# Kernel optimization log

Hardware: AMD Instinct MI355X
Metric: run time of the kernel (lower is better)

Reference implementation:

```python
import jax, jax.numpy as jnp
import numpy as np

D_MODEL = 1024
NHEAD = 16
HEAD_DIM = D_MODEL // NHEAD
MAX_LEN = 4096
ROPE_BASE = 500.0


def _rope_tables(L, dim):
    inv_freq = 1.0 / (ROPE_BASE ** (jnp.arange(0, dim, 2, dtype=jnp.float32) / dim))
    t = jnp.arange(L, dtype=jnp.float32)
    freqs = jnp.einsum('i,j->ij', t, inv_freq)  # [L, dim/2]
    emb = jnp.concatenate([freqs, freqs], axis=-1)  # [L, dim]
    return jnp.cos(emb), jnp.sin(emb)


def _rotate_half(x):
    x1, x2 = jnp.split(x, 2, axis=-1)
    return jnp.concatenate([-x2, x1], axis=-1)


def _apply_rope(x, cos, sin):
    return x * cos + _rotate_half(x) * sin


def setup_inputs() -> dict:
    key = jax.random.key(0)
    ks = jax.random.split(key, 6)
    B, L = 4, 2048
    bound_qkv = 1.0 / np.sqrt(D_MODEL)
    x = jax.random.normal(ks[0], (B, L, D_MODEL), dtype=jnp.float32)
    key_padding_mask = jnp.zeros((B, L), dtype=bool)
    W_qkv = jax.random.uniform(ks[1], (3 * D_MODEL, D_MODEL), jnp.float32, -bound_qkv, bound_qkv)
    b_qkv = jax.random.uniform(ks[2], (3 * D_MODEL,), jnp.float32, -bound_qkv, bound_qkv)
    W_out = jax.random.uniform(ks[3], (D_MODEL, D_MODEL), jnp.float32, -bound_qkv, bound_qkv)
    b_out = jax.random.uniform(ks[4], (D_MODEL,), jnp.float32, -bound_qkv, bound_qkv)
    return {"x": x, "key_padding_mask": key_padding_mask,
            "W_qkv": W_qkv, "b_qkv": b_qkv, "W_out": W_out, "b_out": b_out}


def reference(x, key_padding_mask, W_qkv, b_qkv, W_out, b_out):
    B, L, D = x.shape
    H, hd = NHEAD, HEAD_DIM
    qkv = x @ W_qkv.T + b_qkv  # [B, L, 3D]
    q, k, v = jnp.split(qkv, 3, axis=-1)
    # [B, H, L, hd]
    q = q.reshape(B, L, H, hd).transpose(0, 2, 1, 3)
    k = k.reshape(B, L, H, hd).transpose(0, 2, 1, 3)
    v = v.reshape(B, L, H, hd).transpose(0, 2, 1, 3)
    cos, sin = _rope_tables(L, hd)  # [L, hd]
    q = _apply_rope(q, cos, sin)
    k = _apply_rope(k, cos, sin)
    scores = jnp.einsum('bhqd,bhkd->bhqk', q, k) / jnp.sqrt(jnp.float32(hd))
    mask = key_padding_mask[:, None, None, :]  # [B,1,1,L]
    scores = jnp.where(mask, -jnp.inf, scores)
    attn = jax.nn.softmax(scores, axis=-1)
    out = jnp.einsum('bhqk,bhkd->bhqd', attn, v)
    out = out.transpose(0, 2, 1, 3).reshape(B, L, D)
    return out @ W_out.T + b_out
```

## Files before the change

kernel.cpp:

```cpp
#include <hip/hip_runtime.h>
#include <stdint.h>

typedef __attribute__((ext_vector_type(8))) __bf16 bf16x8;
typedef __attribute__((ext_vector_type(4))) short short4v;
typedef __attribute__((ext_vector_type(4))) float f32x4;

#if __has_builtin(__builtin_amdgcn_exp2f)
#define EXP2(x) __builtin_amdgcn_exp2f(x)
#else
#define EXP2(x) exp2f(x)
#endif

__device__ __forceinline__ short f2bf(float f) {
  union { float f; uint32_t u; } v; v.f = f;
  uint32_t r = (v.u + 0x7fffu + ((v.u >> 16) & 1u)) >> 16;
  return (short)(uint16_t)r;
}

__device__ __forceinline__ uint32_t pk2bf(float a, float b) {
  union { __bf16 h; uint16_t u; } x, y;
  x.h = (__bf16)a; y.h = (__bf16)b;
  return (uint32_t)x.u | ((uint32_t)y.u << 16);
}

__device__ __forceinline__ void gl2lds16(const void* g, const void* lds) {
  __builtin_amdgcn_global_load_lds(
      (const __attribute__((address_space(1))) void*)(uintptr_t)g,
      (__attribute__((address_space(3))) void*)(uint32_t)(uintptr_t)lds,
      16, 0, 0);
}

__device__ __forceinline__ bf16x8 frag8(const short* p) {
  return *(const bf16x8*)(const void*)p;
}

__global__ void convert3_k(const float* __restrict__ s0, short* __restrict__ d0, int n0,
                           const float* __restrict__ s1, short* __restrict__ d1, int n1,
                           const float* __restrict__ s2, short* __restrict__ d2, int n2) {
  int i = blockIdx.x * blockDim.x + threadIdx.x;
  int t0 = n0 >> 2, t1 = t0 + (n1 >> 2), t2 = t1 + (n2 >> 2);
  const float* s; short* d; int off;
  if (i < t0) { s = s0; d = d0; off = i; }
  else if (i < t1) { s = s1; d = d1; off = i - t0; }
  else if (i < t2) { s = s2; d = d2; off = i - t1; }
  else return;
  float4 v = ((const float4*)s)[off];
  short4v o;
  o.x = f2bf(v.x); o.y = f2bf(v.y); o.z = f2bf(v.z); o.w = f2bf(v.w);
  *(short4v*)(d + off * 4) = o;
}

__global__ void rope_tab_k(float* __restrict__ cosT, float* __restrict__ sinT,
                           const unsigned char* __restrict__ mask, float* __restrict__ maskf) {
  int i = blockIdx.x * blockDim.x + threadIdx.x;
  int pos = i >> 5, j = i & 31;
  float invf = exp2f(-(float)j * (8.965784284662087f / 32.0f));
  float ang = (float)pos * invf;
  float s, c;
  sincosf(ang, &s, &c);
  cosT[i] = c; sinT[i] = s;
  if (i < 8192) maskf[i] = mask[i] ? -1e30f : 0.0f;
}

template <int EPI>
__global__ __launch_bounds__(256, 3)
void gemm_bt_k(const short* __restrict__ A, const short* __restrict__ Bm,
               const float* __restrict__ bias, int N, int K,
               float* __restrict__ Cout,
               const float* __restrict__ cosT, const float* __restrict__ sinT,
               short* __restrict__ Qb, short* __restrict__ Kb, short* __restrict__ Vt) {
  __shared__ short As[2][128 * 32];
  __shared__ short Bs[2][128 * 32];
  const int tid = threadIdx.x;
  const int lane = tid & 63;
  const int w = tid >> 6;
  const int g = lane >> 4, l15 = lane & 15;
  const int wm = (w >> 1) * 64, wn = (w & 1) * 64;
  const int bm = blockIdx.x, bn = blockIdx.y;

  const int rseg = lane >> 2;
  const int cofs = ((lane & 3) ^ ((lane >> 3) & 3)) * 8;
  const int sA0 = w, sA1 = w + 4;
  const int arow0 = (bm * 128 + sA0 * 16 + rseg) * K;
  const int arow1 = (bm * 128 + sA1 * 16 + rseg) * K;
  const int brow0 = (bn * 128 + sA0 * 16 + rseg) * K;
  const int brow1 = (bn * 128 + sA1 * 16 + rseg) * K;

  const int rsw = (l15 >> 1) & 3;

  f32x4 acc[4][4];
#pragma unroll
  for (int i = 0; i < 4; i++)
#pragma unroll
    for (int j = 0; j < 4; j++) acc[i][j] = f32x4{0.f, 0.f, 0.f, 0.f};

  gl2lds16(A + arow0 + cofs, &As[0][sA0 * 512]);
  gl2lds16(A + arow1 + cofs, &As[0][sA1 * 512]);
  gl2lds16(Bm + brow0 + cofs, &Bs[0][sA0 * 512]);
  gl2lds16(Bm + brow1 + cofs, &Bs[0][sA1 * 512]);

  int cur = 0;
  for (int k0 = 0; k0 < K; k0 += 32, cur ^= 1) {
    __syncthreads();
    int nxt = cur ^ 1;
    int k1 = k0 + 32;
    if (k1 < K) {
      gl2lds16(A + arow0 + k1 + cofs, &As[nxt][sA0 * 512]);
      gl2lds16(A + arow1 + k1 + cofs, &As[nxt][sA1 * 512]);
      gl2lds16(Bm + brow0 + k1 + cofs, &Bs[nxt][sA0 * 512]);
      gl2lds16(Bm + brow1 + k1 + cofs, &Bs[nxt][sA1 * 512]);
    }
    bf16x8 af[4], bf[4];
#pragma unroll
    for (int im = 0; im < 4; im++) af[im] = frag8(&As[cur][(wm + im * 16 + l15) * 32 + (g ^ rsw) * 8]);
#pragma unroll
    for (int jn = 0; jn < 4; jn++) bf[jn] = frag8(&Bs[cur][(wn + jn * 16 + l15) * 32 + (g ^ rsw) * 8]);
#pragma unroll
    for (int im = 0; im < 4; im++)
#pragma unroll
      for (int jn = 0; jn < 4; jn++)
        acc[im][jn] = __builtin_amdgcn_mfma_f32_16x16x32_bf16(af[im], bf[jn], acc[im][jn], 0, 0, 0);
  }

  const int row0 = bm * 128 + wm + g * 4;
  const int col0 = bn * 128 + wn;

  if (EPI == 0) {
#pragma unroll
    for (int jn = 0; jn < 4; jn++) {
      float bb = bias[col0 + jn * 16 + l15];
#pragma unroll
      for (int im = 0; im < 4; im++)
#pragma unroll
        for (int r = 0; r < 4; r++) {
          int row = row0 + im * 16 + r;
          Cout[row * N + col0 + jn * 16 + l15] = acc[im][jn][r] + bb;
        }
    }
  } else {
#pragma unroll
    for (int jn = 0; jn < 4; jn++) {
      float bb = bias[col0 + jn * 16 + l15];
#pragma unroll
      for (int im = 0; im < 4; im++)
#pragma unroll
        for (int r = 0; r < 4; r++) acc[im][jn][r] += bb;
    }
    const int sector = col0 >> 10;
    const int h = (col0 & 1023) >> 6;
    if (sector == 2) {
#pragma unroll
      for (int jn = 0; jn < 4; jn++) {
        int d = jn * 16 + l15;
#pragma unroll
        for (int im = 0; im < 4; im++) {
          int row = row0 + im * 16;
          int b = row >> 11, pos = row & 2047;
          union { uint32_t u[2]; short4v s4; } pw;
          pw.u[0] = pk2bf(acc[im][jn][0], acc[im][jn][1]);
          pw.u[1] = pk2bf(acc[im][jn][2], acc[im][jn][3]);
          *(short4v*)&Vt[((b * 16 + h) * 64 + d) * 2048 + pos] = pw.s4;
        }
      }
    } else {
      short* dst = (sector == 0) ? Qb : Kb;
      const float scl = (sector == 0) ? 0.18033688011112042f : 1.0f;
#pragma unroll
      for (int jn = 0; jn < 4; jn++) {
        int d = jn * 16 + l15;
        int j = d & 31;
#pragma unroll
        for (int im = 0; im < 4; im++)
#pragma unroll
          for (int r = 0; r < 4; r++) {
            int row = row0 + im * 16 + r;
            int b = row >> 11, pos = row & 2047;
            float c = cosT[pos * 32 + j];
            float s = sinT[pos * 32 + j];
            float xv = acc[im][jn][r];
            float xp = acc[im][jn ^ 2][r];
            float rot = (jn < 2) ? -xp : xp;
            dst[((b * 16 + h) * 2048 + pos) * 64 + d] = f2bf((xv * c + rot * s) * scl);
          }
      }
    }
  }
}

__global__ __launch_bounds__(256, 4)
void attn_k(const short* __restrict__ Qb, const short* __restrict__ Kb,
            const short* __restrict__ Vt, const float* __restrict__ maskf,
            short* __restrict__ attn) {
  __shared__ short Ks[3][32 * 64];
  __shared__ short Vs[3][64 * 32];
  __shared__ short Ps[4][32 * 32];
  __shared__ float Ms[2048];
  const int tid = threadIdx.x, lane = tid & 63, w = tid >> 6;
  const int g = lane >> 4, l15 = lane & 15;
  const int swk = l15 & 7;
  const int fv = (l15 ^ (l15 >> 2)) & 3;
  const int swz = (blockIdx.x & 7) * 128 + (blockIdx.x >> 3);
  const int qt = swz & 15, bh = swz >> 4;
  const int b = bh >> 4, h = bh & 15;

  bf16x8 aq[2][2];
#pragma unroll
  for (int qi = 0; qi < 2; qi++)
#pragma unroll
    for (int kc = 0; kc < 2; kc++) {
      int q = qt * 128 + w * 32 + qi * 16 + l15;
      aq[qi][kc] = *(const bf16x8*)(const void*)(Qb + (bh * 2048 + q) * 64 + kc * 32 + g * 8);
    }
  bf16x8 aone;
#pragma unroll
  for (int i = 0; i < 8; i++) aone[i] = (__bf16)1.0f;

  f32x4 o[4][2];
#pragma unroll
  for (int jd = 0; jd < 4; jd++)
#pragma unroll
    for (int qi = 0; qi < 2; qi++) o[jd][qi] = f32x4{0.f, 0.f, 0.f, 0.f};
  f32x4 lacc[2] = {f32x4{0.f, 0.f, 0.f, 0.f}, f32x4{0.f, 0.f, 0.f, 0.f}};

  bf16x8 av[4], bp[2];
#pragma unroll
  for (int jd = 0; jd < 4; jd++)
#pragma unroll
    for (int i = 0; i < 8; i++) av[jd][i] = (__bf16)0.0f;
#pragma unroll
  for (int qi = 0; qi < 2; qi++)
#pragma unroll
    for (int i = 0; i < 8; i++) bp[qi][i] = (__bf16)0.0f;

  const float* mfp = maskf + b * 2048;

  const int kr8 = lane >> 3;
  const int kcst = (lane & 7) ^ kr8;
  const int vrs = lane >> 2;
  const int vcs = (lane & 3) ^ ((vrs ^ (vrs >> 2)) & 3);

#pragma unroll
  for (int i = 0; i < 2; i++) {
    int s = w * 2 + i;
    gl2lds16(mfp + s * 256 + lane * 4, &Ms[s * 256]);
  }
  if (w < 2) {
#pragma unroll
    for (int t = 0; t < 2; t++)
#pragma unroll
      for (int i = 0; i < 2; i++) {
        int s = (w & 1) * 2 + i;
        gl2lds16(Kb + (bh * 2048 + t * 32 + s * 8 + kr8) * 64 + kcst * 8, &Ks[t][s * 512]);
      }
  } else {
#pragma unroll
    for (int t = 0; t < 2; t++)
#pragma unroll
      for (int i = 0; i < 2; i++) {
        int s = (w & 1) * 2 + i;
        gl2lds16(Vt + (bh * 64 + s * 16 + vrs) * 2048 + t * 32 + vcs * 8, &Vs[t][s * 512]);
      }
  }

  int cur = 0, pre = 2;
  for (int kt = 0; kt < 64; kt++) {
    if (kt < 62) {
      asm volatile("s_waitcnt vmcnt(2)" ::: "memory");
    } else {
      asm volatile("s_waitcnt vmcnt(0)" ::: "memory");
    }
    __builtin_amdgcn_s_barrier();

    if (kt < 62) {
      const int nb = (kt + 2) * 32;
      if (w < 2) {
#pragma unroll
        for (int i = 0; i < 2; i++) {
          int s = (w & 1) * 2 + i;
          gl2lds16(Kb + (bh * 2048 + nb + s * 8 + kr8) * 64 + kcst * 8, &Ks[pre][s * 512]);
        }
      } else {
#pragma unroll
        for (int i = 0; i < 2; i++) {
          int s = (w & 1) * 2 + i;
          gl2lds16(Vt + (bh * 64 + s * 16 + vrs) * 2048 + nb + vcs * 8, &Vs[pre][s * 512]);
        }
      }
    }

    __builtin_amdgcn_s_setprio(1);
#pragma unroll
    for (int qi = 0; qi < 2; qi++) {
#pragma unroll
      for (int jd = 0; jd < 4; jd++)
        o[jd][qi] = __builtin_amdgcn_mfma_f32_16x16x32_bf16(av[jd], bp[qi], o[jd][qi], 0, 0, 0);
      lacc[qi] = __builtin_amdgcn_mfma_f32_16x16x32_bf16(aone, bp[qi], lacc[qi], 0, 0, 0);
    }
    __builtin_amdgcn_s_setprio(0);

    const int kbase = kt * 32;
    f32x4 sv[2][2];
#pragma unroll
    for (int kvt = 0; kvt < 2; kvt++) {
      f32x4 mf = *(const f32x4*)(const void*)&Ms[kbase + kvt * 16 + g * 4];
      sv[kvt][0] = mf; sv[kvt][1] = mf;
    }
    __builtin_amdgcn_s_setprio(1);
#pragma unroll
    for (int kvt = 0; kvt < 2; kvt++)
#pragma unroll
      for (int kc = 0; kc < 2; kc++) {
        bf16x8 ak = frag8(&Ks[cur][(kvt * 16 + l15) * 64 + ((kc * 4 + g) ^ swk) * 8]);
        sv[kvt][0] = __builtin_amdgcn_mfma_f32_16x16x32_bf16(ak, aq[0][kc], sv[kvt][0], 0, 0, 0);
        sv[kvt][1] = __builtin_amdgcn_mfma_f32_16x16x32_bf16(ak, aq[1][kc], sv[kvt][1], 0, 0, 0);
      }
    __builtin_amdgcn_s_setprio(0);

#pragma unroll
    for (int jd = 0; jd < 4; jd++)
      av[jd] = frag8(&Vs[cur][(jd * 16 + l15) * 32 + (g ^ fv) * 8]);

#pragma unroll
    for (int qi = 0; qi < 2; qi++)
#pragma unroll
      for (int kvt = 0; kvt < 2; kvt++) {
        union { uint32_t u[2]; short4v s4; } pw;
        pw.u[0] = pk2bf(EXP2(sv[kvt][qi][0]), EXP2(sv[kvt][qi][1]));
        pw.u[1] = pk2bf(EXP2(sv[kvt][qi][2]), EXP2(sv[kvt][qi][3]));
        *(short4v*)&Ps[w][(qi * 16 + l15) * 32 + (((kvt * 2 + (g >> 1)) ^ fv) * 8) + (g & 1) * 4] = pw.s4;
      }
#pragma unroll
    for (int qi = 0; qi < 2; qi++)
      bp[qi] = frag8(&Ps[w][(qi * 16 + l15) * 32 + (g ^ fv) * 8]);

    cur = (cur == 2) ? 0 : cur + 1;
    pre = (pre == 2) ? 0 : pre + 1;
  }

  __builtin_amdgcn_s_setprio(1);
#pragma unroll
  for (int qi = 0; qi < 2; qi++) {
#pragma unroll
    for (int jd = 0; jd < 4; jd++)
      o[jd][qi] = __builtin_amdgcn_mfma_f32_16x16x32_bf16(av[jd], bp[qi], o[jd][qi], 0, 0, 0);
    lacc[qi] = __builtin_amdgcn_mfma_f32_16x16x32_bf16(aone, bp[qi], lacc[qi], 0, 0, 0);
  }
  __builtin_amdgcn_s_setprio(0);

#pragma unroll
  for (int qi = 0; qi < 2; qi++) {
    float inv = 1.0f / lacc[qi][0];
    int q = qt * 128 + w * 32 + qi * 16 + l15;
#pragma unroll
    for (int jd = 0; jd < 4; jd++) {
      union { uint32_t u[2]; short4v s4; } pw;
      pw.u[0] = pk2bf(o[jd][qi][0] * inv, o[jd][qi][1] * inv);
      pw.u[1] = pk2bf(o[jd][qi][2] * inv, o[jd][qi][3] * inv);
      *(short4v*)&attn[(b * 2048 + q) * 1024 + h * 64 + jd * 16 + g * 4] = pw.s4;
    }
  }
}

extern "C" void kernel_launch(void* const* d_in, const int* in_sizes, int n_in,
                              void* d_out, int out_size, void* d_ws, size_t ws_size,
                              hipStream_t stream) {
  const float* x = (const float*)d_in[0];
  const unsigned char* mask = (const unsigned char*)d_in[1];
  const float* W_qkv = (const float*)d_in[2];
  const float* b_qkv = (const float*)d_in[3];
  const float* W_out = (const float*)d_in[4];
  const float* b_out = (const float*)d_in[5];
  float* out = (float*)d_out;

  char* ws = (char*)d_ws;
  short* xb    = (short*)(ws + 0);
  short* wqkvb = (short*)(ws + 16777216);
  short* woutb = (short*)(ws + 23068672);
  float* cosT  = (float*)(ws + 25165824);
  float* sinT  = (float*)(ws + 25427968);
  short* Qb    = (short*)(ws + 25690112);
  short* Kb    = (short*)(ws + 42467328);
  short* Vtb   = (short*)(ws + 59244544);
  short* attnb = (short*)(ws + 76021760);
  float* maskf = (float*)(ws + 92798976);

  convert3_k<<<12288, 256, 0, stream>>>(x, xb, 8388608, W_qkv, wqkvb, 3145728, W_out, woutb, 1048576);
  rope_tab_k<<<256, 256, 0, stream>>>(cosT, sinT, mask, maskf);
  gemm_bt_k<1><<<dim3(64, 24), 256, 0, stream>>>(xb, wqkvb, b_qkv, 3072, 1024,
                                                 nullptr, cosT, sinT, Qb, Kb, Vtb);
  attn_k<<<dim3(1024), 256, 0, stream>>>(Qb, Kb, Vtb, maskf, attnb);
  gemm_bt_k<0><<<dim3(64, 8), 256, 0, stream>>>(attnb, woutb, b_out, 1024, 1024,
                                                out, nullptr, nullptr, nullptr, nullptr, nullptr);
}
```

Baseline: 282.9 us.

## Load V fragments directly from global and shuffle P in registers via permlane swaps

V tiles are no longer staged through LDS. Each lane reads its V^T fragments straight from global memory into registers, and the K staging is redistributed evenly across all four waves. The P matrix transpose through shared memory is replaced by v_permlane32/16_swap instructions that rearrange the bf16-packed exponentials across lanes into the MFMA B-operand layout. This drops an LDS write, a read and LDS footprint per tile, which may raise occupancy. In exchange, V latency is exposed to global/L2 loads with deeper vmcnt waits, and the code depends on the lane-permutation mapping being correct.

```diff
diff --git a/kernel.cpp b/kernel.cpp
--- a/kernel.cpp
+++ b/kernel.cpp
@@ -4,6 +4,7 @@
 typedef __attribute__((ext_vector_type(8))) __bf16 bf16x8;
 typedef __attribute__((ext_vector_type(4))) short short4v;
 typedef __attribute__((ext_vector_type(4))) float f32x4;
+typedef __attribute__((ext_vector_type(4))) uint32_t u32x4;
 
 #if __has_builtin(__builtin_amdgcn_exp2f)
 #define EXP2(x) __builtin_amdgcn_exp2f(x)
@@ -192,13 +193,10 @@
             const short* __restrict__ Vt, const float* __restrict__ maskf,
             short* __restrict__ attn) {
   __shared__ short Ks[3][32 * 64];
-  __shared__ short Vs[3][64 * 32];
-  __shared__ short Ps[4][32 * 32];
   __shared__ float Ms[2048];
   const int tid = threadIdx.x, lane = tid & 63, w = tid >> 6;
   const int g = lane >> 4, l15 = lane & 15;
   const int swk = l15 & 7;
-  const int fv = (l15 ^ (l15 >> 2)) & 3;
   const int swz = (blockIdx.x & 7) * 128 + (blockIdx.x >> 3);
   const int qt = swz & 15, bh = swz >> 4;
   const int b = bh >> 4, h = bh & 15;
@@ -236,56 +234,27 @@
 
   const int kr8 = lane >> 3;
   const int kcst = (lane & 7) ^ kr8;
-  const int vrs = lane >> 2;
-  const int vcs = (lane & 3) ^ ((vrs ^ (vrs >> 2)) & 3);
+  const short* vbase = Vt + ((size_t)(bh * 64 + l15)) * 2048 + g * 8;
 
 #pragma unroll
   for (int i = 0; i < 2; i++) {
     int s = w * 2 + i;
     gl2lds16(mfp + s * 256 + lane * 4, &Ms[s * 256]);
   }
-  if (w < 2) {
-#pragma unroll
-    for (int t = 0; t < 2; t++)
-#pragma unroll
-      for (int i = 0; i < 2; i++) {
-        int s = (w & 1) * 2 + i;
-        gl2lds16(Kb + (bh * 2048 + t * 32 + s * 8 + kr8) * 64 + kcst * 8, &Ks[t][s * 512]);
-      }
-  } else {
-#pragma unroll
-    for (int t = 0; t < 2; t++)
-#pragma unroll
-      for (int i = 0; i < 2; i++) {
-        int s = (w & 1) * 2 + i;
-        gl2lds16(Vt + (bh * 64 + s * 16 + vrs) * 2048 + t * 32 + vcs * 8, &Vs[t][s * 512]);
-      }
-  }
+#pragma unroll
+  for (int t = 0; t < 2; t++)
+    gl2lds16(Kb + (bh * 2048 + t * 32 + w * 8 + kr8) * 64 + kcst * 8, &Ks[t][w * 512]);
 
   int cur = 0, pre = 2;
   for (int kt = 0; kt < 64; kt++) {
-    if (kt < 62) {
-      asm volatile("s_waitcnt vmcnt(2)" ::: "memory");
-    } else {
-      asm volatile("s_waitcnt vmcnt(0)" ::: "memory");
-    }
+    if (kt == 0)      { asm volatile("s_waitcnt vmcnt(0)" ::: "memory"); }
+    else if (kt < 63) { asm volatile("s_waitcnt vmcnt(5)" ::: "memory"); }
+    else              { asm volatile("s_waitcnt vmcnt(4)" ::: "memory"); }
     __builtin_amdgcn_s_barrier();
 
     if (kt < 62) {
       const int nb = (kt + 2) * 32;
-      if (w < 2) {
-#pragma unroll
-        for (int i = 0; i < 2; i++) {
-          int s = (w & 1) * 2 + i;
-          gl2lds16(Kb + (bh * 2048 + nb + s * 8 + kr8) * 64 + kcst * 8, &Ks[pre][s * 512]);
-        }
-      } else {
-#pragma unroll
-        for (int i = 0; i < 2; i++) {
-          int s = (w & 1) * 2 + i;
-          gl2lds16(Vt + (bh * 64 + s * 16 + vrs) * 2048 + nb + vcs * 8, &Vs[pre][s * 512]);
-        }
-      }
+      gl2lds16(Kb + (bh * 2048 + nb + w * 8 + kr8) * 64 + kcst * 8, &Ks[pre][w * 512]);
     }
 
     __builtin_amdgcn_s_setprio(1);
@@ -297,6 +266,13 @@
       lacc[qi] = __builtin_amdgcn_mfma_f32_16x16x32_bf16(aone, bp[qi], lacc[qi], 0, 0, 0);
     }
     __builtin_amdgcn_s_setprio(0);
+
+    {
+      const short* vp = vbase + kt * 32;
+#pragma unroll
+      for (int jd = 0; jd < 4; jd++)
+        av[jd] = frag8(vp + jd * 16 * 2048);
+    }
 
     const int kbase = kt * 32;
     f32x4 sv[2][2];
@@ -317,21 +293,19 @@
     __builtin_amdgcn_s_setprio(0);
 
 #pragma unroll
-    for (int jd = 0; jd < 4; jd++)
-      av[jd] = frag8(&Vs[cur][(jd * 16 + l15) * 32 + (g ^ fv) * 8]);
-
-#pragma unroll
-    for (int qi = 0; qi < 2; qi++)
-#pragma unroll
-      for (int kvt = 0; kvt < 2; kvt++) {
-        union { uint32_t u[2]; short4v s4; } pw;
-        pw.u[0] = pk2bf(EXP2(sv[kvt][qi][0]), EXP2(sv[kvt][qi][1]));
-        pw.u[1] = pk2bf(EXP2(sv[kvt][qi][2]), EXP2(sv[kvt][qi][3]));
-        *(short4v*)&Ps[w][(qi * 16 + l15) * 32 + (((kvt * 2 + (g >> 1)) ^ fv) * 8) + (g & 1) * 4] = pw.s4;
-      }
-#pragma unroll
-    for (int qi = 0; qi < 2; qi++)
-      bp[qi] = frag8(&Ps[w][(qi * 16 + l15) * 32 + (g ^ fv) * 8]);
+    for (int qi = 0; qi < 2; qi++) {
+      uint32_t x0 = pk2bf(EXP2(sv[0][qi][0]), EXP2(sv[0][qi][1]));
+      uint32_t x1 = pk2bf(EXP2(sv[0][qi][2]), EXP2(sv[0][qi][3]));
+      uint32_t y0 = pk2bf(EXP2(sv[1][qi][0]), EXP2(sv[1][qi][1]));
+      uint32_t y1 = pk2bf(EXP2(sv[1][qi][2]), EXP2(sv[1][qi][3]));
+      asm("v_permlane32_swap_b32 %0, %1" : "+v"(x0), "+v"(y0));
+      asm("v_permlane16_swap_b32 %0, %1" : "+v"(x0), "+v"(y0));
+      asm("v_permlane32_swap_b32 %0, %1" : "+v"(x1), "+v"(y1));
+      asm("v_permlane16_swap_b32 %0, %1" : "+v"(x1), "+v"(y1));
+      union { u32x4 u; bf16x8 f; } pb;
+      pb.u = u32x4{x0, x1, y0, y1};
+      bp[qi] = pb.f;
+    }
 
     cur = (cur == 2) ? 0 : cur + 1;
     pre = (pre == 2) ? 0 : pre + 1;
```

After: 327.1 us. +15.6%, slower.

## Triple-buffer GEMM LDS tiles with explicit vmcnt waits for deeper prefetch

Applied to the files above, without the earlier changes.

Grows the GEMM shared-memory staging from two to three buffers and prefetches two K-tiles ahead. The plain __syncthreads is replaced by partial s_waitcnt vmcnt(4) plus s_barrier, so only the oldest tile's loads must land before compute. This hides more global-load latency, but LDS use rises from 32KB to 48KB per block, which may cut occupancy under launch_bounds(256,3). The vmcnt-based ordering also relies on exact counts of outstanding loads.

```diff
diff --git a/kernel.cpp b/kernel.cpp
--- a/kernel.cpp
+++ b/kernel.cpp
@@ -69,8 +69,8 @@
                float* __restrict__ Cout,
                const float* __restrict__ cosT, const float* __restrict__ sinT,
                short* __restrict__ Qb, short* __restrict__ Kb, short* __restrict__ Vt) {
-  __shared__ short As[2][128 * 32];
-  __shared__ short Bs[2][128 * 32];
+  __shared__ short As[3][128 * 32];
+  __shared__ short Bs[3][128 * 32];
   const int tid = threadIdx.x;
   const int lane = tid & 63;
   const int w = tid >> 6;
@@ -94,21 +94,27 @@
 #pragma unroll
     for (int j = 0; j < 4; j++) acc[i][j] = f32x4{0.f, 0.f, 0.f, 0.f};
 
-  gl2lds16(A + arow0 + cofs, &As[0][sA0 * 512]);
-  gl2lds16(A + arow1 + cofs, &As[0][sA1 * 512]);
-  gl2lds16(Bm + brow0 + cofs, &Bs[0][sA0 * 512]);
-  gl2lds16(Bm + brow1 + cofs, &Bs[0][sA1 * 512]);
-
-  int cur = 0;
-  for (int k0 = 0; k0 < K; k0 += 32, cur ^= 1) {
-    __syncthreads();
-    int nxt = cur ^ 1;
-    int k1 = k0 + 32;
-    if (k1 < K) {
-      gl2lds16(A + arow0 + k1 + cofs, &As[nxt][sA0 * 512]);
-      gl2lds16(A + arow1 + k1 + cofs, &As[nxt][sA1 * 512]);
-      gl2lds16(Bm + brow0 + k1 + cofs, &Bs[nxt][sA0 * 512]);
-      gl2lds16(Bm + brow1 + k1 + cofs, &Bs[nxt][sA1 * 512]);
+#pragma unroll
+  for (int t = 0; t < 2; t++) {
+    gl2lds16(A + arow0 + t * 32 + cofs, &As[t][sA0 * 512]);
+    gl2lds16(A + arow1 + t * 32 + cofs, &As[t][sA1 * 512]);
+    gl2lds16(Bm + brow0 + t * 32 + cofs, &Bs[t][sA0 * 512]);
+    gl2lds16(Bm + brow1 + t * 32 + cofs, &Bs[t][sA1 * 512]);
+  }
+
+  const int K32 = K >> 5;
+  int cur = 0, pre = 2;
+  for (int kt = 0; kt < K32; kt++) {
+    if (kt < K32 - 1) { asm volatile("s_waitcnt vmcnt(4)" ::: "memory"); }
+    else              { asm volatile("s_waitcnt vmcnt(0)" ::: "memory"); }
+    __builtin_amdgcn_s_barrier();
+
+    if (kt + 2 < K32) {
+      const int k2 = (kt + 2) * 32;
+      gl2lds16(A + arow0 + k2 + cofs, &As[pre][sA0 * 512]);
+      gl2lds16(A + arow1 + k2 + cofs, &As[pre][sA1 * 512]);
+      gl2lds16(Bm + brow0 + k2 + cofs, &Bs[pre][sA0 * 512]);
+      gl2lds16(Bm + brow1 + k2 + cofs, &Bs[pre][sA1 * 512]);
     }
     bf16x8 af[4], bf[4];
 #pragma unroll
@@ -120,6 +126,9 @@
 #pragma unroll
       for (int jn = 0; jn < 4; jn++)
         acc[im][jn] = __builtin_amdgcn_mfma_f32_16x16x32_bf16(af[im], bf[jn], acc[im][jn], 0, 0, 0);
+
+    cur = (cur == 2) ? 0 : cur + 1;
+    pre = (pre == 2) ? 0 : pre + 1;
   }
 
   const int row0 = bm * 128 + wm + g * 4;
```

Result: faster. 275.8 us (-2.5%).
